# Performance work log

Measured on AMD Instinct MI355X. Metric: run time of the kernel, lower is better.

The kernel has to match this reference:

```python
import jax, jax.numpy as jnp
import numpy as np

# module hyperparameters (init_kwargs)
HIDDEN = 256
NUM_BLOCKS = 8
BLOCK = HIDDEN // NUM_BLOCKS  # 32
HSF = 1                       # hidden_size_factor
LAMBDA = 0.01                 # sparsity_threshold (softshrink)
FRAC = 1.0                    # hard_thresholding_fraction
SCALE = 0.02


def setup_inputs() -> dict:
    key = jax.random.key(0)
    ks = jax.random.split(key, 5)
    B, D, H, W, C = 2, 16, 64, 64, HIDDEN
    x = jax.random.normal(ks[0], (B, D, H, W, C), dtype=jnp.float32)
    w1 = SCALE * jax.random.normal(ks[1], (2, NUM_BLOCKS, BLOCK, BLOCK * HSF), dtype=jnp.float32)
    b1 = SCALE * jax.random.normal(ks[2], (2, NUM_BLOCKS, BLOCK * HSF), dtype=jnp.float32)
    w2 = SCALE * jax.random.normal(ks[3], (2, NUM_BLOCKS, BLOCK * HSF, BLOCK), dtype=jnp.float32)
    b2 = SCALE * jax.random.normal(ks[4], (2, NUM_BLOCKS, BLOCK), dtype=jnp.float32)
    return {"x": x, "w1": w1, "b1": b1, "w2": w2, "b2": b2}


def _softshrink(v):
    return jnp.where(v > LAMBDA, v - LAMBDA, jnp.where(v < -LAMBDA, v + LAMBDA, jnp.zeros_like(v)))


def _block_cmul(ar, ai, w):
    # complex block-diagonal matmul: (ar + i*ai) @ (w[0] + i*w[1])
    rr = jnp.einsum('bdhwni,nio->bdhwno', ar, w[0]) - jnp.einsum('bdhwni,nio->bdhwno', ai, w[1])
    ii = jnp.einsum('bdhwni,nio->bdhwno', ai, w[0]) + jnp.einsum('bdhwni,nio->bdhwno', ar, w[1])
    return rr, ii


def _fft3d(x, w1, b1, w2, b2):
    bias = x
    B, D, H, W, C = x.shape
    xf = jnp.fft.rfftn(x.astype(jnp.float32), axes=(1, 2, 3), norm='ortho')
    Wf = W // 2 + 1
    xf = xf.reshape(B, D, H, Wf, NUM_BLOCKS, BLOCK)

    total_modes = H // 2 + 1
    kept = int(total_modes * FRAC)
    h_lo, h_hi = total_modes - kept, min(total_modes + kept, H)  # torch slicing clips
    w_hi = min(kept, Wf)

    xs = xf[:, :, h_lo:h_hi, :w_hi]           # kept modes only
    xr, xi = jnp.real(xs), jnp.imag(xs)

    # layer 1: complex block MLP + bias + relu (applied to real/imag separately)
    r1, i1 = _block_cmul(xr, xi, w1)
    r1 = jax.nn.relu(r1 + b1[0])
    i1 = jax.nn.relu(i1 + b1[1])

    # layer 2: complex block MLP + bias
    r2, i2 = _block_cmul(r1, i1, w2)
    r2 = r2 + b2[0]
    i2 = i2 + b2[1]

    # softshrink on real and imag parts (softshrink(0)=0 so zero-padding unchanged)
    r2 = _softshrink(r2)
    i2 = _softshrink(i2)

    out_f = jnp.zeros((B, D, H, Wf, NUM_BLOCKS, BLOCK), dtype=jnp.complex64)
    out_f = out_f.at[:, :, h_lo:h_hi, :w_hi].set(r2 + 1j * i2)
    out_f = out_f.reshape(B, D, H, Wf, C)

    out = jnp.fft.irfftn(out_f, s=(D, H, W), axes=(1, 2, 3), norm='ortho')
    return out.astype(x.dtype) + bias


def reference(x, w1, b1, w2, b2):
    return _fft3d(x, w1, b1, w2, b2)
```

## Files before the change

### kernel.cpp

```cpp
#include <hip/hip_runtime.h>
#include <math.h>

#define BB 2
#define DD 16
#define HH 64
#define WW 64
#define WF 33
#define CC 256

typedef __attribute__((ext_vector_type(8))) short bf16x8;
typedef __attribute__((ext_vector_type(4))) float f32x4;
typedef __attribute__((ext_vector_type(4))) unsigned int u32x4;

__device__ __forceinline__ unsigned short f2bf(float f) {
    unsigned u = __builtin_bit_cast(unsigned int, f);
    u += 0x7fffu + ((u >> 16) & 1u);
    return (unsigned short)(u >> 16);
}

__device__ __forceinline__ bf16x8 bneg(bf16x8 a) {
    u32x4 u = __builtin_bit_cast(u32x4, a);
    u = u ^ 0x80008000u;
    return __builtin_bit_cast(bf16x8, u);
}

__device__ __forceinline__ float2 cmul(float2 a, float2 b) {
    return make_float2(a.x * b.x - a.y * b.y, a.x * b.y + a.y * b.x);
}

template <int N, bool INV>
__device__ __forceinline__ void cfft(float2* v) {
    constexpr int L = (N == 64) ? 6 : (N == 32) ? 5 : (N == 16) ? 4 : 0;
    static_assert(L > 0, "unsupported N");
#pragma unroll
    for (int i = 0; i < N; ++i) {
        int j = 0;
#pragma unroll
        for (int bpos = 0; bpos < L; ++bpos) j |= ((i >> bpos) & 1) << (L - 1 - bpos);
        if (j > i) { float2 t = v[i]; v[i] = v[j]; v[j] = t; }
    }
#pragma unroll
    for (int s = 1; s <= L; ++s) {
        const int m = 1 << s;
#pragma unroll
        for (int k = 0; k < N; k += m) {
#pragma unroll
            for (int j = 0; j < m / 2; ++j) {
                float ang = (INV ? 2.0f : -2.0f) * 3.14159265358979323846f * (float)j / (float)m;
                float ss, cc;
                __sincosf(ang, &ss, &cc);
                float2 w = make_float2(cc, ss);
                float2 u = v[k + j];
                float2 t = cmul(w, v[k + j + m / 2]);
                v[k + j]         = make_float2(u.x + t.x, u.y + t.y);
                v[k + j + m / 2] = make_float2(u.x - t.x, u.y - t.y);
            }
        }
    }
}

__global__ __launch_bounds__(256) void kA(const float* __restrict__ x, float2* __restrict__ spec) {
    const int t = threadIdx.x;
    const int h = blockIdx.x * 2 + (t >> 7);
    const int d = blockIdx.y, b = blockIdx.z;
    const int cp = t & 127;
    const float2* px = (const float2*)(x + (((size_t)(b * DD + d) * HH + h) * WW) * CC) + cp;
    float2 u[WW];
#pragma unroll
    for (int w = 0; w < WW; ++w) u[w] = px[(size_t)w * (CC / 2)];
    cfft<64, false>(u);
    float2* ps = spec + (((size_t)(b * DD + d) * HH + h) * WF) * CC + 2 * cp;
    const float s = 0.5f / 256.0f;
#pragma unroll
    for (int k = 0; k < WF; ++k) {
        float2 p = u[k];
        float2 q = u[(64 - k) & 63];
        float4 o;
        o.x = (p.x + q.x) * s;
        o.y = (p.y - q.y) * s;
        o.z = (p.y + q.y) * s;
        o.w = (q.x - p.x) * s;
        *(float4*)(ps + (size_t)k * CC) = o;
    }
}

template <bool INV>
__global__ __launch_bounds__(256) void kH(float2* __restrict__ spec) {
    const int wf = blockIdx.x, d = blockIdx.y, b = blockIdx.z, c = threadIdx.x;
    float2* ps = spec + (((size_t)(b * DD + d) * HH) * WF + wf) * CC + c;
    const size_t sh = (size_t)WF * CC;
    float2 v[HH];
#pragma unroll
    for (int h = 0; h < HH; ++h) v[h] = ps[(size_t)h * sh];
    cfft<64, INV>(v);
#pragma unroll
    for (int h = 0; h < HH; ++h) ps[(size_t)h * sh] = v[h];
}

__device__ __forceinline__ float softshrink(float v) {
    return (v > 0.01f) ? v - 0.01f : ((v < -0.01f) ? v + 0.01f : 0.0f);
}

__global__ __launch_bounds__(256) void kC(float2* __restrict__ spec,
                                          const float* __restrict__ w1, const float* __restrict__ b1,
                                          const float* __restrict__ w2, const float* __restrict__ b2) {
    const int wf = blockIdx.x, h = blockIdx.y, b = blockIdx.z;
    const int c = threadIdx.x;
    const int wv = c >> 6, lane = c & 63;
    const int lrow = lane & 15, lgrp = lane >> 4;

    __shared__ __align__(16) unsigned char smem[32768];

    float2* ps = spec + (((size_t)b * DD * HH + h) * WF + wf) * CC + c;
    const size_t sd = (size_t)HH * WF * CC;

    float b1r_[2][2], b1i_[2][2], b2r_[2][2], b2i_[2][2];
#pragma unroll
    for (int nb = 0; nb < 2; ++nb) {
        const int n = 2 * wv + nb;
#pragma unroll
        for (int t = 0; t < 2; ++t) {
            const int ob = n * 32 + t * 16 + lrow;
            b1r_[nb][t] = b1[ob];  b1i_[nb][t] = b1[256 + ob];
            b2r_[nb][t] = b2[ob];  b2i_[nb][t] = b2[256 + ob];
        }
    }

    bf16x8 Wr[2][2], Wi[2][2];
#pragma unroll
    for (int nb = 0; nb < 2; ++nb) {
        const int n = 2 * wv + nb;
#pragma unroll
        for (int t = 0; t < 2; ++t) {
            const int col = t * 16 + lrow;
#pragma unroll
            for (int j = 0; j < 8; ++j) {
                const int k = lgrp * 8 + j;
                Wr[nb][t][j] = (short)f2bf(w1[n * 1024 + k * 32 + col]);
                Wi[nb][t][j] = (short)f2bf(w1[8192 + n * 1024 + k * 32 + col]);
            }
        }
    }

    float2 v[DD];
#pragma unroll
    for (int d = 0; d < DD; ++d) v[d] = ps[(size_t)d * sd];
    cfft<16, false>(v);

    {
        const int n = c >> 5, in = c & 31;
        unsigned short* Ar = (unsigned short*)smem;
#pragma unroll
        for (int d = 0; d < DD; ++d) {
            Ar[n * 512 + d * 32 + in]        = f2bf(v[d].x);
            Ar[4096 + n * 512 + d * 32 + in] = f2bf(v[d].y);
        }
    }
    __syncthreads();

    const f32x4 zero = {0.f, 0.f, 0.f, 0.f};

#pragma unroll
    for (int nb = 0; nb < 2; ++nb) {
        const int n = 2 * wv + nb;
        const int abase = n * 1024 + lrow * 64 + lgrp * 16;
        bf16x8 xr  = *(const bf16x8*)(smem + abase);
        bf16x8 xi  = *(const bf16x8*)(smem + 8192 + abase);
        bf16x8 nxi = bneg(xi);
        unsigned short* H = (unsigned short*)(smem + 16384);
#pragma unroll
        for (int t = 0; t < 2; ++t) {
            f32x4 rr = __builtin_amdgcn_mfma_f32_16x16x32_bf16(xr, Wr[nb][t], zero, 0, 0, 0);
            rr = __builtin_amdgcn_mfma_f32_16x16x32_bf16(nxi, Wi[nb][t], rr, 0, 0, 0);
            f32x4 ii = __builtin_amdgcn_mfma_f32_16x16x32_bf16(xi, Wr[nb][t], zero, 0, 0, 0);
            ii = __builtin_amdgcn_mfma_f32_16x16x32_bf16(xr, Wi[nb][t], ii, 0, 0, 0);
            const int hcol = n * 512 + (t * 16 + lrow);
#pragma unroll
            for (int r = 0; r < 4; ++r) {
                const int d = lgrp * 4 + r;
                H[hcol + d * 32]        = f2bf(fmaxf(rr[r] + b1r_[nb][t], 0.f));
                H[4096 + hcol + d * 32] = f2bf(fmaxf(ii[r] + b1i_[nb][t], 0.f));
            }
        }
    }
    __syncthreads();

#pragma unroll
    for (int nb = 0; nb < 2; ++nb) {
        const int n = 2 * wv + nb;
#pragma unroll
        for (int t = 0; t < 2; ++t) {
            const int col = t * 16 + lrow;
#pragma unroll
            for (int j = 0; j < 8; ++j) {
                const int k = lgrp * 8 + j;
                Wr[nb][t][j] = (short)f2bf(w2[n * 1024 + k * 32 + col]);
                Wi[nb][t][j] = (short)f2bf(w2[8192 + n * 1024 + k * 32 + col]);
            }
        }
    }

    f32x4 arr[2][2], aii[2][2];
#pragma unroll
    for (int nb = 0; nb < 2; ++nb) {
        const int n = 2 * wv + nb;
        const int hbase = 16384 + n * 1024 + lrow * 64 + lgrp * 16;
        bf16x8 hr  = *(const bf16x8*)(smem + hbase);
        bf16x8 hi  = *(const bf16x8*)(smem + 8192 + hbase);
        bf16x8 nhi = bneg(hi);
#pragma unroll
        for (int t = 0; t < 2; ++t) {
            f32x4 rr = __builtin_amdgcn_mfma_f32_16x16x32_bf16(hr, Wr[nb][t], zero, 0, 0, 0);
            rr = __builtin_amdgcn_mfma_f32_16x16x32_bf16(nhi, Wi[nb][t], rr, 0, 0, 0);
            f32x4 ii = __builtin_amdgcn_mfma_f32_16x16x32_bf16(hi, Wr[nb][t], zero, 0, 0, 0);
            ii = __builtin_amdgcn_mfma_f32_16x16x32_bf16(hr, Wi[nb][t], ii, 0, 0, 0);
            arr[nb][t] = rr;  aii[nb][t] = ii;
        }
    }
    __syncthreads();

    float2* FO = (float2*)smem;
#pragma unroll
    for (int nb = 0; nb < 2; ++nb) {
        const int n = 2 * wv + nb;
#pragma unroll
        for (int t = 0; t < 2; ++t) {
            const int co = n * 32 + t * 16 + lrow;
#pragma unroll
            for (int r = 0; r < 4; ++r) {
                const int d = lgrp * 4 + r;
                FO[d * 256 + co] = make_float2(softshrink(arr[nb][t][r] + b2r_[nb][t]),
                                               softshrink(aii[nb][t][r] + b2i_[nb][t]));
            }
        }
    }
    __syncthreads();

#pragma unroll
    for (int d = 0; d < DD; ++d) v[d] = FO[d * 256 + c];
    cfft<16, true>(v);
#pragma unroll
    for (int d = 0; d < DD; ++d) ps[(size_t)d * sd] = v[d];
}

__global__ __launch_bounds__(256) void kE(const float2* __restrict__ spec, const float* __restrict__ x,
                                          float* __restrict__ out) {
    const int h = blockIdx.x, d = blockIdx.y, b = blockIdx.z, c = threadIdx.x;
    const float2* ps = spec + (((size_t)(b * DD + d) * HH + h) * WF) * CC + c;
    float2 v[WW];
#pragma unroll
    for (int k = 0; k < WF; ++k) v[k] = ps[(size_t)k * CC];
#pragma unroll
    for (int k = WF; k < WW; ++k) { float2 t = v[WW - k]; v[k] = make_float2(t.x, -t.y); }
    cfft<64, true>(v);
    const size_t xb = (((size_t)(b * DD + d) * HH + h) * WW) * CC + c;
#pragma unroll
    for (int w = 0; w < WW; ++w) {
        out[xb + (size_t)w * CC] = v[w].x * (1.0f / 256.0f) + x[xb + (size_t)w * CC];
    }
}

extern "C" void kernel_launch(void* const* d_in, const int* in_sizes, int n_in,
                              void* d_out, int out_size, void* d_ws, size_t ws_size,
                              hipStream_t stream) {
    const float* x  = (const float*)d_in[0];
    const float* w1 = (const float*)d_in[1];
    const float* b1 = (const float*)d_in[2];
    const float* w2 = (const float*)d_in[3];
    const float* b2 = (const float*)d_in[4];
    float* out = (float*)d_out;
    float2* spec = (float2*)d_ws;

    dim3 blk(256);
    kA<<<dim3(HH / 2, DD, BB), blk, 0, stream>>>(x, spec);
    kH<false><<<dim3(WF, DD, BB), blk, 0, stream>>>(spec);
    kC<<<dim3(WF, HH, BB), blk, 0, stream>>>(spec, w1, b1, w2, b2);
    kH<true><<<dim3(WF, DD, BB), blk, 0, stream>>>(spec);
    kE<<<dim3(HH, DD, BB), blk, 0, stream>>>(spec, x, out);
}
```

Measured before the change: 278.8 us.

## Pack two real channels into one complex inverse FFT along W

The final inverse W-axis transform now runs one complex 64-point FFT per pair of channels. Each thread loads the Hermitian half-spectra of two channels and combines them as X1 + i*X2, rebuilding the full spectrum, so the real and imaginary outputs give the two channels' real signals. This halves the FFT work and the grid size and widens the loads and stores to float4 and float2. In exchange, each thread does more index arithmetic and there are fewer blocks to keep the GPU busy.

```diff
diff --git a/kernel.cpp b/kernel.cpp
--- a/kernel.cpp
+++ b/kernel.cpp
@@ -245,18 +245,36 @@
 
 __global__ __launch_bounds__(256) void kE(const float2* __restrict__ spec, const float* __restrict__ x,
                                           float* __restrict__ out) {
-    const int h = blockIdx.x, d = blockIdx.y, b = blockIdx.z, c = threadIdx.x;
-    const float2* ps = spec + (((size_t)(b * DD + d) * HH + h) * WF) * CC + c;
+    const int t = threadIdx.x;
+    const int h = blockIdx.x * 2 + (t >> 7);
+    const int d = blockIdx.y, b = blockIdx.z;
+    const int cp = t & 127;
+    const float2* ps = spec + (((size_t)(b * DD + d) * HH + h) * WF) * CC + 2 * cp;
+
     float2 v[WW];
-#pragma unroll
-    for (int k = 0; k < WF; ++k) v[k] = ps[(size_t)k * CC];
-#pragma unroll
-    for (int k = WF; k < WW; ++k) { float2 t = v[WW - k]; v[k] = make_float2(t.x, -t.y); }
+    {
+        float4 q = *(const float4*)(ps);
+        v[0] = make_float2(q.x, q.z);
+    }
+    {
+        float4 q = *(const float4*)(ps + (size_t)32 * CC);
+        v[32] = make_float2(q.x, q.z);
+    }
+#pragma unroll
+    for (int k = 1; k < 32; ++k) {
+        float4 q = *(const float4*)(ps + (size_t)k * CC);
+        v[k]      = make_float2(q.x - q.w, q.y + q.z);
+        v[64 - k] = make_float2(q.x + q.w, q.z - q.y);
+    }
     cfft<64, true>(v);
-    const size_t xb = (((size_t)(b * DD + d) * HH + h) * WW) * CC + c;
+
+    const float2* px = (const float2*)(x + (((size_t)(b * DD + d) * HH + h) * WW) * CC) + cp;
+    float2* po = (float2*)(out + (((size_t)(b * DD + d) * HH + h) * WW) * CC) + cp;
+    const float s = 1.0f / 256.0f;
 #pragma unroll
     for (int w = 0; w < WW; ++w) {
-        out[xb + (size_t)w * CC] = v[w].x * (1.0f / 256.0f) + x[xb + (size_t)w * CC];
+        float2 xb = px[(size_t)w * (CC / 2)];
+        po[(size_t)w * (CC / 2)] = make_float2(v[w].x * s + xb.x, v[w].y * s + xb.y);
     }
 }
 
@@ -276,5 +294,5 @@
     kH<false><<<dim3(WF, DD, BB), blk, 0, stream>>>(spec);
     kC<<<dim3(WF, HH, BB), blk, 0, stream>>>(spec, w1, b1, w2, b2);
     kH<true><<<dim3(WF, DD, BB), blk, 0, stream>>>(spec);
-    kE<<<dim3(HH, DD, BB), blk, 0, stream>>>(spec, x, out);
-}
+    kE<<<dim3(HH / 2, DD, BB), blk, 0, stream>>>(spec, x, out);
+}
```

Result: slower. 329.6 us (+18.2%).
